# Optimization experiments

Measured on AMD Instinct MI355X. Metric: run time of the kernel, lower is better.

Reference implementation:

```python
import jax, jax.numpy as jnp
import numpy as np

B, T, D = 1, 2048, 1024
H = 16
HD = D // H
K = 4
FF = 4 * D
LAYERS = 24
EPS = 1.1920929e-07  # torch.finfo(float32).eps, RMSNorm default


def setup_inputs() -> dict:
    key = jax.random.key(0)
    ks = jax.random.split(key, 16)
    s = 0.02
    return {
        "x": jax.random.normal(ks[0], (B, T, D), jnp.float32),
        "gamma": jax.random.uniform(ks[1], (D,), jnp.float32),
        "beta": jax.random.normal(ks[2], (D,), jnp.float32) * 0.1,
        "iter_scale": jax.random.uniform(ks[3], (1,), jnp.float32),
        "qkv_bases": jax.random.normal(ks[4], (K, 3 * D, D), jnp.float32) * s,
        "o_bases": jax.random.normal(ks[5], (K, D, D), jnp.float32) * s,
        "gate_bases": jax.random.normal(ks[6], (K, FF, D), jnp.float32) * s,
        "up_bases": jax.random.normal(ks[7], (K, FF, D), jnp.float32) * s,
        "down_bases": jax.random.normal(ks[8], (K, D, FF), jnp.float32) * s,
        "alpha_qkv": jax.random.normal(ks[9], (LAYERS, K), jnp.float32) * 0.1 + jnp.eye(LAYERS, K)[:, :K] * 0.0 + jnp.concatenate([jnp.ones((LAYERS, 1)), jnp.zeros((LAYERS, K - 1))], axis=1),
        "alpha_o": jnp.concatenate([jnp.ones((LAYERS, 1)), jnp.zeros((LAYERS, K - 1))], axis=1) + jax.random.normal(ks[10], (LAYERS, K)) * 0.1,
        "alpha_gate": jnp.concatenate([jnp.ones((LAYERS, 1)), jnp.zeros((LAYERS, K - 1))], axis=1) + jax.random.normal(ks[11], (LAYERS, K)) * 0.1,
        "alpha_up": jnp.concatenate([jnp.ones((LAYERS, 1)), jnp.zeros((LAYERS, K - 1))], axis=1) + jax.random.normal(ks[12], (LAYERS, K)) * 0.1,
        "alpha_down": jnp.concatenate([jnp.ones((LAYERS, 1)), jnp.zeros((LAYERS, K - 1))], axis=1) + jax.random.normal(ks[13], (LAYERS, K)) * 0.1,
        "norm1_w": jnp.ones((D,), jnp.float32),
        "norm2_w": jnp.ones((D,), jnp.float32),
        "layer_idx": 5,
    }


def _rmsnorm(x, w):
    return x * jax.lax.rsqrt(jnp.mean(x * x, axis=-1, keepdims=True) + EPS) * w


def reference(x, gamma, beta, iter_scale, qkv_bases, o_bases, gate_bases, up_bases,
              down_bases, alpha_qkv, alpha_o, alpha_gate, alpha_up, alpha_down,
              norm1_w, norm2_w, layer_idx):
    Bx, Tx, Dx = x.shape
    # --- attention sub-block ---
    h = _rmsnorm(x, norm1_w) * gamma + beta
    W_qkv = jnp.einsum('k,kij->ij', alpha_qkv[layer_idx], qkv_bases)  # [3D, D]
    qkv = jnp.einsum('btd,od->bto', h, W_qkv).reshape(Bx, Tx, 3, H, HD)
    qkv = jnp.transpose(qkv, (2, 0, 3, 1, 4))  # [3, B, H, T, HD]
    q, k, v = qkv[0], qkv[1], qkv[2]
    scores = jnp.einsum('bhqd,bhkd->bhqk', q, k) / jnp.sqrt(jnp.asarray(HD, x.dtype))
    causal = jnp.tril(jnp.ones((Tx, Tx), bool))
    scores = jnp.where(causal, scores, jnp.asarray(-jnp.inf, scores.dtype))
    attn = jax.nn.softmax(scores, axis=-1)
    out = jnp.einsum('bhqk,bhkd->bhqd', attn, v)
    out = jnp.transpose(out, (0, 2, 1, 3)).reshape(Bx, Tx, Dx)
    W_o = jnp.einsum('k,kij->ij', alpha_o[layer_idx], o_bases)
    x_attn = x + jnp.einsum('btd,od->bto', out, W_o)
    # --- SwiGLU FFN sub-block ---
    h2 = _rmsnorm(x_attn, norm2_w) * gamma + beta
    W_g = jnp.einsum('k,kij->ij', alpha_gate[layer_idx], gate_bases)
    W_u = jnp.einsum('k,kij->ij', alpha_up[layer_idx], up_bases)
    W_d = jnp.einsum('k,kij->ij', alpha_down[layer_idx], down_bases)
    gate = jnp.einsum('btd,fd->btf', h2, W_g)
    up = jnp.einsum('btd,fd->btf', h2, W_u)
    ffn_out = jnp.einsum('btf,df->btd', jax.nn.silu(gate) * up, W_d)
    block_out = x_attn + ffn_out
    return x + (block_out - x) * iter_scale
```

## Files before the change

kernel.cpp:

```cpp
#include <hip/hip_runtime.h>
#include <hip/hip_bf16.h>
#include <math.h>

typedef __bf16 bf16;
typedef __bf16 bf16x8 __attribute__((ext_vector_type(8)));
typedef __bf16 bf16x4 __attribute__((ext_vector_type(4)));
typedef float f32x4 __attribute__((ext_vector_type(4)));

#define EPSc 1.1920929e-07f
#define LOG2E 1.44269504f

static __device__ __forceinline__ void glds16(const void* g, void* l) {
  __builtin_amdgcn_global_load_lds((const __attribute__((address_space(1))) void*)g,
                                   (__attribute__((address_space(3))) void*)l, 16, 0, 0);
}

static __device__ __forceinline__ bf16x4 comb4(const float* b0, const float* b1,
                                               const float* b2, const float* b3,
                                               float a0, float a1, float a2, float a3) {
  float4 v0 = *(const float4*)b0, v1 = *(const float4*)b1;
  float4 v2 = *(const float4*)b2, v3 = *(const float4*)b3;
  bf16x4 o;
  o[0] = (bf16)(a0*v0.x + a1*v1.x + a2*v2.x + a3*v3.x);
  o[1] = (bf16)(a0*v0.y + a1*v1.y + a2*v2.y + a3*v3.y);
  o[2] = (bf16)(a0*v0.z + a1*v1.z + a2*v2.z + a3*v3.z);
  o[3] = (bf16)(a0*v0.w + a1*v1.w + a2*v2.w + a3*v3.w);
  return o;
}

__global__ __launch_bounds__(256)
void prep1(const float* __restrict__ qkv_b, const float* __restrict__ a_qkv,
           const float* __restrict__ o_b,   const float* __restrict__ a_o,
           const float* __restrict__ x, const float* __restrict__ n1w,
           const float* __restrict__ gamma, const float* __restrict__ beta,
           const int* __restrict__ lidx,
           bf16* __restrict__ Wqkv, bf16* __restrict__ Wo, bf16* __restrict__ hbuf) {
  const int bid = blockIdx.x, tid = threadIdx.x;
  if (bid < 4096) {
    int li = lidx[0];
    const float* base; const float* al; bf16* out; size_t flat, n;
    if (bid < 3072) { base = qkv_b; al = a_qkv; out = Wqkv; flat = (size_t)bid << 10; n = (size_t)3072*1024; }
    else            { base = o_b;   al = a_o;   out = Wo;   flat = (size_t)(bid-3072) << 10; n = (size_t)1024*1024; }
    float a0 = al[li*4], a1 = al[li*4+1], a2 = al[li*4+2], a3 = al[li*4+3];
    size_t off = flat + tid*4;
    bf16x4 o = comb4(base+off, base+n+off, base+2*n+off, base+3*n+off, a0, a1, a2, a3);
    *(bf16x4*)&out[off] = o;
  } else {
    int row = bid - 4096, t = tid;
    const float4* xr = (const float4*)(x + (size_t)row*1024);
    float4 v = xr[t];
    float ss = v.x*v.x + v.y*v.y + v.z*v.z + v.w*v.w;
    #pragma unroll
    for (int off = 32; off > 0; off >>= 1) ss += __shfl_down(ss, off, 64);
    __shared__ float red[4];
    if ((t & 63) == 0) red[t >> 6] = ss;
    __syncthreads();
    float tot = red[0] + red[1] + red[2] + red[3];
    float r = rsqrtf(tot * (1.0f/1024.0f) + EPSc);
    float4 wv = ((const float4*)n1w)[t];
    float4 gv = ((const float4*)gamma)[t];
    float4 bv = ((const float4*)beta)[t];
    bf16x4 o;
    o[0] = (bf16)(v.x*r*wv.x*gv.x + bv.x);
    o[1] = (bf16)(v.y*r*wv.y*gv.y + bv.y);
    o[2] = (bf16)(v.z*r*wv.z*gv.z + bv.z);
    o[3] = (bf16)(v.w*r*wv.w*gv.w + bv.w);
    *(bf16x4*)&hbuf[(size_t)row*1024 + t*4] = o;
  }
}

__global__ __launch_bounds__(256) void rmsnorm_k(const float* __restrict__ x,
                                                 const float* __restrict__ w,
                                                 const float* __restrict__ gamma,
                                                 const float* __restrict__ beta,
                                                 bf16* __restrict__ out) {
  int row = blockIdx.x, t = threadIdx.x;
  const float4* xr = (const float4*)(x + (size_t)row*1024);
  float4 v = xr[t];
  float ss = v.x*v.x + v.y*v.y + v.z*v.z + v.w*v.w;
  #pragma unroll
  for (int off = 32; off > 0; off >>= 1) ss += __shfl_down(ss, off, 64);
  __shared__ float red[4];
  if ((t & 63) == 0) red[t >> 6] = ss;
  __syncthreads();
  float tot = red[0] + red[1] + red[2] + red[3];
  float r = rsqrtf(tot * (1.0f/1024.0f) + EPSc);
  float4 wv = ((const float4*)w)[t];
  float4 gv = ((const float4*)gamma)[t];
  float4 bv = ((const float4*)beta)[t];
  bf16x4 o;
  o[0] = (bf16)(v.x*r*wv.x*gv.x + bv.x);
  o[1] = (bf16)(v.y*r*wv.y*gv.y + bv.y);
  o[2] = (bf16)(v.z*r*wv.z*gv.z + bv.z);
  o[3] = (bf16)(v.w*r*wv.w*gv.w + bv.w);
  *(bf16x4*)&out[(size_t)row*1024 + t*4] = o;
}

template<int EP, int NTW>
__global__ __launch_bounds__(256)
void gemm_bt(const bf16* __restrict__ A, const bf16* __restrict__ Bw,
             int M, int N, int K, int lda, int ldb, int gx,
             float* __restrict__ outf, bf16* __restrict__ outb,
             const float* __restrict__ auxf, const float* __restrict__ auxf2,
             const float* __restrict__ iscale) {
  constexpr int BN = NTW * 32;
  __shared__ __align__(16) bf16 As[2][128*64];
  __shared__ __align__(16) bf16 Bs[2][BN*64];
  const int nwg = gridDim.x;
  const int orig = blockIdx.x;
  const int wg = (orig & 7) * (nwg >> 3) + (orig >> 3);
  const int tn0 = (wg % gx) * BN, tm0 = (wg / gx) * 128;
  const int tid = threadIdx.x, wave = tid >> 6, lane = tid & 63;
  const int lr = lane & 15, lg = lane >> 4;
  const int wr = wave >> 1, wc = wave & 1;
  f32x4 acc[4][NTW] = {};
  const int rs = lane >> 3;
  const int sc = (((lane & 7) ^ rs) << 3);
  const int x0 = ((lg ^ (lr & 7)) << 3);
  const int x1 = (((4 + lg) ^ (lr & 7)) << 3);

  const bf16* Abase = A + (size_t)tm0 * lda;
  const bf16* Bbase = Bw + (size_t)tn0 * ldb;

  auto stage = [&](bf16* as, bf16* bs, int k0) {
    #pragma unroll
    for (int j = 0; j < 4; ++j) {
      int chunk = wave*4 + j;
      int r = chunk*8 + rs;
      glds16(Abase + (size_t)r*lda + k0 + sc, as + chunk*512 + lane*8);
    }
    #pragma unroll
    for (int j = 0; j < NTW; ++j) {
      int chunk = wave*NTW + j;
      int r = chunk*8 + rs;
      glds16(Bbase + (size_t)r*ldb + k0 + sc, bs + chunk*512 + lane*8);
    }
  };
  auto comp = [&](const bf16* as, const bf16* bs) {
    #pragma unroll
    for (int kk = 0; kk < 2; ++kk) {
      const int x = kk ? x1 : x0;
      bf16x8 av[4], bv[NTW];
      #pragma unroll
      for (int m = 0; m < 4; ++m) av[m] = *(const bf16x8*)&as[(wr*64 + m*16 + lr)*64 + x];
      #pragma unroll
      for (int n = 0; n < NTW; ++n) bv[n] = *(const bf16x8*)&bs[(wc*NTW*16 + n*16 + lr)*64 + x];
      #pragma unroll
      for (int m = 0; m < 4; ++m)
        #pragma unroll
        for (int n = 0; n < NTW; ++n)
          acc[m][n] = __builtin_amdgcn_mfma_f32_16x16x32_bf16(av[m], bv[n], acc[m][n], 0, 0, 0);
    }
  };

  bf16 *a0 = As[0], *a1 = As[1], *b0 = Bs[0], *b1 = Bs[1];
  stage(a0, b0, 0);
  __syncthreads();
  for (int k0 = 64; k0 < K; k0 += 64) {
    stage(a1, b1, k0);
    comp(a0, b0);
    __syncthreads();
    bf16* t;
    t = a0; a0 = a1; a1 = t;
    t = b0; b0 = b1; b1 = t;
  }
  comp(a0, b0);

  float its = 0.f;
  if constexpr (EP == 4) its = iscale[0];
  #pragma unroll
  for (int m = 0; m < 4; ++m)
    #pragma unroll
    for (int n = 0; n < NTW; ++n)
      #pragma unroll
      for (int i = 0; i < 4; ++i) {
        int row = tm0 + wr*64 + m*16 + lg*4 + i;
        int col = tn0 + wc*NTW*16 + n*16 + lr;
        size_t idx = (size_t)row * N + col;
        float v = acc[m][n][i];
        if constexpr (EP == 0) outb[idx] = (bf16)v;
        else if constexpr (EP == 1) outf[idx] = auxf[idx] + v;
        else if constexpr (EP == 4) {
          float xv = auxf[idx], xa = auxf2[idx];
          outf[idx] = xv + (xa + v - xv) * its;
        }
      }
}

__global__ __launch_bounds__(512, 2)
void gemm_gu256(const bf16* __restrict__ A, const bf16* __restrict__ Bw,
                bf16* __restrict__ outb) {
  __shared__ __align__(16) bf16 L[2][2][2][8192];
  const int orig = blockIdx.x;
  const int wg = (orig & 7) * 32 + (orig >> 3);
  const int tn0 = (wg & 31) * 256, tm0 = (wg >> 5) * 256;
  const int tid = threadIdx.x, wave = tid >> 6, lane = tid & 63;
  const int lr = lane & 15, lg = lane >> 4;
  const int wr = wave >> 2, wn = wave & 3;
  const int rs8 = lane >> 3;
  const int gc8 = (((lane & 7) ^ rs8) << 3);
  const int xk0 = ((lg ^ (lr & 7)) << 3);
  const int xk1 = (((4 + lg) ^ (lr & 7)) << 3);
  f32x4 acc[8][4] = {};

  const bf16* Ab = A + (size_t)tm0 * 1024;
  const bf16* Bb = Bw + (size_t)tn0 * 1024;

  auto stage_half = [&](bf16* dst, const bf16* gbase, int half, int k0) {
    #pragma unroll
    for (int l = 0; l < 2; ++l) {
      int r = half*128 + (wave*2 + l)*8 + rs8;
      glds16(gbase + (size_t)r*1024 + k0 + gc8, dst + (wave*2 + l)*512 + lane*8);
    }
  };

  stage_half(&L[0][0][0][0], Ab, 0, 0);
  stage_half(&L[0][0][1][0], Ab, 1, 0);
  stage_half(&L[0][1][0][0], Bb, 0, 0);
  stage_half(&L[0][1][1][0], Bb, 1, 0);
  stage_half(&L[1][1][0][0], Bb, 0, 64);
  stage_half(&L[1][1][1][0], Bb, 1, 64);
  asm volatile("s_waitcnt vmcnt(4)" ::: "memory");
  __builtin_amdgcn_s_barrier();

  for (int t = 0; t < 16; ++t) {
    const int b = t & 1;
    const bf16* ah = &L[b][0][wr][0];
    const bf16* bh = &L[b][1][wn >> 1][0];
    bf16x8 breg[4][2];
    #pragma unroll
    for (int p = 0; p < 4; ++p) {
      if (p == 0) {
        #pragma unroll
        for (int n = 0; n < 4; ++n) {
          int row = (wn & 1)*64 + n*16 + lr;
          breg[n][0] = *(const bf16x8*)&bh[row*64 + xk0];
          breg[n][1] = *(const bf16x8*)&bh[row*64 + xk1];
        }
      }
      bf16x8 av[2][2];
      #pragma unroll
      for (int mi = 0; mi < 2; ++mi) {
        int row = p*32 + mi*16 + lr;
        av[mi][0] = *(const bf16x8*)&ah[row*64 + xk0];
        av[mi][1] = *(const bf16x8*)&ah[row*64 + xk1];
      }
      if (p == 0 && t < 15) stage_half(&L[b^1][0][0][0], Ab, 0, (t+1)*64);
      if (p == 1 && t < 15) stage_half(&L[b^1][0][1][0], Ab, 1, (t+1)*64);
      if (p == 2 && t < 14) stage_half(&L[b][1][0][0], Bb, 0, (t+2)*64);
      if (p == 3 && t < 14) stage_half(&L[b][1][1][0], Bb, 1, (t+2)*64);
      __builtin_amdgcn_s_barrier();
      __builtin_amdgcn_s_setprio(1);
      #pragma unroll
      for (int mi = 0; mi < 2; ++mi)
        #pragma unroll
        for (int n = 0; n < 4; ++n) {
          acc[p*2+mi][n] = __builtin_amdgcn_mfma_f32_16x16x32_bf16(av[mi][0], breg[n][0], acc[p*2+mi][n], 0, 0, 0);
          acc[p*2+mi][n] = __builtin_amdgcn_mfma_f32_16x16x32_bf16(av[mi][1], breg[n][1], acc[p*2+mi][n], 0, 0, 0);
        }
      __builtin_amdgcn_s_setprio(0);
      if (p == 3) {
        if (t >= 14) asm volatile("s_waitcnt vmcnt(0)" ::: "memory");
        else         asm volatile("s_waitcnt vmcnt(4)" ::: "memory");
      }
      __builtin_amdgcn_s_barrier();
    }
  }

  #pragma unroll
  for (int mf = 0; mf < 8; ++mf)
    #pragma unroll
    for (int j = 0; j < 2; ++j)
      #pragma unroll
      for (int i = 0; i < 4; ++i) {
        int row = tm0 + wr*128 + mf*16 + lg*4 + i;
        int col = (tn0 >> 1) + wn*32 + j*16 + lr;
        float g = acc[mf][2*j][i], u = acc[mf][2*j+1][i];
        float s = g / (1.f + __builtin_amdgcn_exp2f(-g * LOG2E));
        outb[(size_t)row * 4096 + col] = (bf16)(s * u);
      }
}

__global__ __launch_bounds__(256)
void attn_mega(const bf16* __restrict__ qkv, bf16* __restrict__ out,
               const float* __restrict__ gate_b, const float* __restrict__ up_b,
               const float* __restrict__ down_b,
               const float* __restrict__ a_gate, const float* __restrict__ a_up,
               const float* __restrict__ a_down, const int* __restrict__ lidx,
               bf16* __restrict__ Wgu, bf16* __restrict__ Wd) {
  __shared__ __align__(16) bf16 Ks[2][64*72];
  __shared__ __align__(16) bf16 Vt[2][64*66];
  __shared__ __align__(16) bf16 Ps[4][2][16*72];
  const int bid = blockIdx.x;
  const int tid = threadIdx.x;

  if (bid < 256) {
    const int cb = bid;
    int li = lidx[0];
    float g0 = a_gate[li*4], g1 = a_gate[li*4+1], g2 = a_gate[li*4+2], g3 = a_gate[li*4+3];
    float u0 = a_up[li*4],   u1 = a_up[li*4+1],   u2 = a_up[li*4+2],   u3 = a_up[li*4+3];
    float d0 = a_down[li*4], d1 = a_down[li*4+1], d2 = a_down[li*4+2], d3 = a_down[li*4+3];
    const size_t PS = (size_t)4096 * 1024;
    for (int it = 0; it < 48; ++it) {
      int chunk = it * 256 + cb;
      if (chunk < 8192) {
        int r = chunk, w = r & 31;
        int f = ((r >> 5) << 4) + (w & 15);
        const float* base = (w < 16) ? gate_b : up_b;
        float a0 = (w < 16) ? g0 : u0, a1 = (w < 16) ? g1 : u1;
        float a2 = (w < 16) ? g2 : u2, a3 = (w < 16) ? g3 : u3;
        size_t src = (size_t)f*1024 + tid*4;
        bf16x4 o = comb4(base+src, base+PS+src, base+2*PS+src, base+3*PS+src, a0, a1, a2, a3);
        *(bf16x4*)&Wgu[((size_t)r << 10) + tid*4] = o;
      } else {
        size_t off = ((size_t)(chunk - 8192) << 10) + tid*4;
        bf16x4 o = comb4(down_b+off, down_b+PS+off, down_b+2*PS+off, down_b+3*PS+off, d0, d1, d2, d3);
        *(bf16x4*)&Wd[off] = o;
      }
    }
    return;
  }

  const int a = bid - 256;
  const int qb = 15 - (a >> 4);
  const int h = a & 15;
  const int wave = tid >> 6, lane = tid & 63;
  const int lr = lane & 15, lg = lane >> 4;
  const int q0 = qb * 128;
  const int qw = q0 + wave * 32;

  bf16x8 qf[2][2];
  #pragma unroll
  for (int qt = 0; qt < 2; ++qt) {
    const bf16* qrow = qkv + (size_t)(qw + qt*16 + lr)*3072 + h*64;
    qf[qt][0] = *(const bf16x8*)(qrow + lg*8);
    qf[qt][1] = *(const bf16x8*)(qrow + 32 + lg*8);
  }
  f32x4 o[2][4] = {};
  float mrow[2], lrow[2];
  mrow[0] = mrow[1] = -__builtin_inff();
  lrow[0] = lrow[1] = 0.f;
  const int xsrc = (lane & 48) | (lg << 2);

  const int r0 = tid >> 3, r1 = r0 + 32;
  const int c0 = (tid & 7) << 3;
  const bf16* kb = qkv + 1024 + h*64 + c0;
  const bf16* vb = qkv + 2048 + h*64 + c0;

  bf16x8 kreg[2], vreg[2];
  auto stage_load = [&](int kv0) {
    kreg[0] = *(const bf16x8*)(kb + (size_t)(kv0 + r0)*3072);
    kreg[1] = *(const bf16x8*)(kb + (size_t)(kv0 + r1)*3072);
    vreg[0] = *(const bf16x8*)(vb + (size_t)(kv0 + r0)*3072);
    vreg[1] = *(const bf16x8*)(vb + (size_t)(kv0 + r1)*3072);
  };
  auto stage_write = [&](int buf) {
    *(bf16x8*)&Ks[buf][r0*72 + c0] = kreg[0];
    *(bf16x8*)&Ks[buf][r1*72 + c0] = kreg[1];
    #pragma unroll
    for (int e = 0; e < 8; ++e) Vt[buf][(c0 + e)*66 + r0] = vreg[0][e];
    #pragma unroll
    for (int e = 0; e < 8; ++e) Vt[buf][(c0 + e)*66 + r1] = vreg[1][e];
  };

  stage_load(0);
  stage_write(0);
  __syncthreads();
  int cur = 0;

  const float C = 0.125f * LOG2E;
  const int nt = 2 * (qb + 1);

  for (int t = 0; t < nt; ++t) {
    const int kv0 = t * 64;
    if (t < nt-1) stage_load(kv0 + 64);

    f32x4 s[2][4] = {};
    __builtin_amdgcn_s_setprio(1);
    #pragma unroll
    for (int n = 0; n < 4; ++n) {
      bf16x8 k0f = *(const bf16x8*)&Ks[cur][(n*16 + lr)*72 + lg*8];
      bf16x8 k1f = *(const bf16x8*)&Ks[cur][(n*16 + lr)*72 + 32 + lg*8];
      #pragma unroll
      for (int qt = 0; qt < 2; ++qt) {
        s[qt][n] = __builtin_amdgcn_mfma_f32_16x16x32_bf16(k0f, qf[qt][0], s[qt][n], 0, 0, 0);
        s[qt][n] = __builtin_amdgcn_mfma_f32_16x16x32_bf16(k1f, qf[qt][1], s[qt][n], 0, 0, 0);
      }
    }
    __builtin_amdgcn_s_setprio(0);

    if (kv0 + 63 > qw) {
      #pragma unroll
      for (int qt = 0; qt < 2; ++qt) {
        const int qv = qw + qt*16 + lr;
        #pragma unroll
        for (int n = 0; n < 4; ++n)
          #pragma unroll
          for (int i = 0; i < 4; ++i)
            if (kv0 + n*16 + lg*4 + i > qv) s[qt][n][i] = -__builtin_inff();
      }
    }

    float pmn[2];
    #pragma unroll
    for (int qt = 0; qt < 2; ++qt) {
      f32x4 t0 = s[qt][0], t1 = s[qt][1];
      #pragma unroll
      for (int i = 0; i < 4; ++i) { t0[i] = fmaxf(t0[i], s[qt][2][i]); t1[i] = fmaxf(t1[i], s[qt][3][i]); }
      float a0 = fmaxf(t0[0], t0[1]), a1 = fmaxf(t0[2], t0[3]);
      float b0 = fmaxf(t1[0], t1[1]), b1 = fmaxf(t1[2], t1[3]);
      float mnew = fmaxf(fmaxf(a0, a1), fmaxf(b0, b1));
      mnew = fmaxf(mnew, __shfl_xor(mnew, 16, 64));
      mnew = fmaxf(mnew, __shfl_xor(mnew, 32, 64));
      pmn[qt] = mnew * C;
    }
    bool grow = (pmn[0] > mrow[0] + 8.f) || (pmn[1] > mrow[1] + 8.f);
    if (__any(grow)) {
      #pragma unroll
      for (int qt = 0; qt < 2; ++qt) {
        float mt = fmaxf(mrow[qt], pmn[qt]);
        float fc = __builtin_amdgcn_exp2f(mrow[qt] - mt);
        mrow[qt] = mt;
        lrow[qt] *= fc;
        #pragma unroll
        for (int i = 0; i < 4; ++i) {
          float fci = __shfl(fc, xsrc + i, 64);
          #pragma unroll
          for (int nd = 0; nd < 4; ++nd) o[qt][nd][i] *= fci;
        }
      }
    }
    #pragma unroll
    for (int qt = 0; qt < 2; ++qt) {
      float mref = fmaxf(mrow[qt], -3e38f);
      float rsum = 0.f;
      #pragma unroll
      for (int n = 0; n < 4; ++n) {
        bf16x4 p4;
        #pragma unroll
        for (int i = 0; i < 4; ++i) {
          float e = __builtin_amdgcn_exp2f(__builtin_fmaf(s[qt][n][i], C, -mref));
          rsum += e;
          p4[i] = (bf16)e;
        }
        *(bf16x4*)&Ps[wave][qt][lr*72 + n*16 + lg*4] = p4;
      }
      rsum += __shfl_xor(rsum, 16, 64);
      rsum += __shfl_xor(rsum, 32, 64);
      lrow[qt] += rsum;
    }
    asm volatile("s_waitcnt lgkmcnt(0)" ::: "memory");

    #pragma unroll
    for (int kk = 0; kk < 2; ++kk) {
      bf16x8 pf0 = *(const bf16x8*)&Ps[wave][0][lr*72 + kk*32 + lg*8];
      bf16x8 pf1 = *(const bf16x8*)&Ps[wave][1][lr*72 + kk*32 + lg*8];
      __builtin_amdgcn_s_setprio(1);
      #pragma unroll
      for (int nd = 0; nd < 4; ++nd) {
        bf16x8 vf = *(const bf16x8*)&Vt[cur][(nd*16 + lr)*66 + kk*32 + lg*8];
        o[0][nd] = __builtin_amdgcn_mfma_f32_16x16x32_bf16(pf0, vf, o[0][nd], 0, 0, 0);
        o[1][nd] = __builtin_amdgcn_mfma_f32_16x16x32_bf16(pf1, vf, o[1][nd], 0, 0, 0);
      }
      __builtin_amdgcn_s_setprio(0);
    }
    if (t < nt-1) {
      stage_write(cur ^ 1);
      __syncthreads();
      cur ^= 1;
    }
  }
  #pragma unroll
  for (int qt = 0; qt < 2; ++qt)
    #pragma unroll
    for (int i = 0; i < 4; ++i) {
      float li = __shfl(lrow[qt], xsrc + i, 64);
      float inv = 1.f / li;
      #pragma unroll
      for (int nd = 0; nd < 4; ++nd)
        out[(size_t)(qw + qt*16 + lg*4 + i)*1024 + h*64 + nd*16 + lr] = (bf16)(o[qt][nd][i]*inv);
    }
}

extern "C" void kernel_launch(void* const* d_in, const int* in_sizes, int n_in,
                              void* d_out, int out_size, void* d_ws, size_t ws_size,
                              hipStream_t stream) {
  const float* x        = (const float*)d_in[0];
  const float* gamma    = (const float*)d_in[1];
  const float* beta     = (const float*)d_in[2];
  const float* iscale   = (const float*)d_in[3];
  const float* qkv_b    = (const float*)d_in[4];
  const float* o_b      = (const float*)d_in[5];
  const float* gate_b   = (const float*)d_in[6];
  const float* up_b     = (const float*)d_in[7];
  const float* down_b   = (const float*)d_in[8];
  const float* a_qkv    = (const float*)d_in[9];
  const float* a_o      = (const float*)d_in[10];
  const float* a_gate   = (const float*)d_in[11];
  const float* a_up     = (const float*)d_in[12];
  const float* a_down   = (const float*)d_in[13];
  const float* n1w      = (const float*)d_in[14];
  const float* n2w      = (const float*)d_in[15];
  const int*   lidx     = (const int*)d_in[16];

  char* p = (char*)d_ws;
  auto alloc = [&](size_t bytes) { char* r = p; p += (bytes + 255) & ~(size_t)255; return r; };
  bf16*  Wqkv = (bf16*)alloc((size_t)3072*1024*2);
  bf16*  Wo   = (bf16*)alloc((size_t)1024*1024*2);
  bf16*  Wgu  = (bf16*)alloc((size_t)8192*1024*2);
  bf16*  Wd   = (bf16*)alloc((size_t)1024*4096*2);
  bf16*  hbuf = (bf16*)alloc((size_t)2048*1024*2);
  bf16*  qkvb = (bf16*)alloc((size_t)2048*3072*2);
  bf16*  attn = (bf16*)alloc((size_t)2048*1024*2);
  float* xat  = (float*)alloc((size_t)2048*1024*4);
  bf16*  h2   = (bf16*)alloc((size_t)2048*1024*2);
  bf16*  act  = (bf16*)alloc((size_t)2048*4096*2);
  float* out  = (float*)d_out;

  prep1<<<6144, 256, 0, stream>>>(qkv_b, a_qkv, o_b, a_o, x, n1w, gamma, beta, lidx,
                                  Wqkv, Wo, hbuf);
  gemm_bt<0,4><<<24*16, 256, 0, stream>>>(hbuf, Wqkv, 2048, 3072, 1024, 1024, 1024, 24,
                                          nullptr, qkvb, nullptr, nullptr, nullptr);
  attn_mega<<<512, 256, 0, stream>>>(qkvb, attn, gate_b, up_b, down_b,
                                     a_gate, a_up, a_down, lidx, Wgu, Wd);
  gemm_bt<1,2><<<16*16, 256, 0, stream>>>(attn, Wo, 2048, 1024, 1024, 1024, 1024, 16,
                                          xat, nullptr, x, nullptr, nullptr);
  rmsnorm_k<<<2048, 256, 0, stream>>>(xat, n2w, gamma, beta, h2);
  gemm_gu256<<<256, 512, 0, stream>>>(h2, Wgu, act);
  gemm_bt<4,2><<<16*16, 256, 0, stream>>>(act, Wd, 2048, 1024, 4096, 4096, 4096, 16,
                                          out, nullptr, x, xat, iscale);
}
```

Measured before the change: 201.7 us.

## Split causal attention KV range in two and merge partials in new kernel

Each attention (query-block, head) work item is split into two halves of the key/value range, doubling the attention block count so heavy causal query blocks are spread over more CUs. Each half writes unnormalised fp32 outputs plus its running max and sum, and a new merge kernel combines them into the bf16 attention output. The P tile stride in LDS also changes from 72 to 68, which changes the bank mapping. In exchange this adds an extra launch and fp32 partial traffic of roughly 16 MB written and read back, and the split is even in tiles rather than in causal work.

```diff
diff --git a/kernel.cpp b/kernel.cpp
--- a/kernel.cpp
+++ b/kernel.cpp
@@ -282,15 +282,41 @@
 }
 
 __global__ __launch_bounds__(256)
-void attn_mega(const bf16* __restrict__ qkv, bf16* __restrict__ out,
+void attn_merge(const float* __restrict__ oPart, const float* __restrict__ mPart,
+                const float* __restrict__ lPart, bf16* __restrict__ out) {
+  const int q = blockIdx.x, tid = threadIdx.x;
+  const int h = tid >> 4;
+  const size_t HQ = (size_t)16 * 2048;
+  float mA = mPart[h*2048 + q],      mB = mPart[HQ + h*2048 + q];
+  float lA = lPart[h*2048 + q],      lB = lPart[HQ + h*2048 + q];
+  float fm = fmaxf(mA, mB);
+  float eA = __builtin_amdgcn_exp2f(mA - fm);
+  float eB = __builtin_amdgcn_exp2f(mB - fm);
+  float inv = 1.f / (lA*eA + lB*eB);
+  const size_t QD = (size_t)2048 * 1024;
+  size_t idx = (size_t)q*1024 + tid*4;
+  float4 oA = *(const float4*)&oPart[idx];
+  float4 oB = *(const float4*)&oPart[QD + idx];
+  bf16x4 o;
+  o[0] = (bf16)((oA.x*eA + oB.x*eB) * inv);
+  o[1] = (bf16)((oA.y*eA + oB.y*eB) * inv);
+  o[2] = (bf16)((oA.z*eA + oB.z*eB) * inv);
+  o[3] = (bf16)((oA.w*eA + oB.w*eB) * inv);
+  *(bf16x4*)&out[idx] = o;
+}
+
+__global__ __launch_bounds__(256)
+void attn_mega(const bf16* __restrict__ qkv,
                const float* __restrict__ gate_b, const float* __restrict__ up_b,
                const float* __restrict__ down_b,
                const float* __restrict__ a_gate, const float* __restrict__ a_up,
                const float* __restrict__ a_down, const int* __restrict__ lidx,
-               bf16* __restrict__ Wgu, bf16* __restrict__ Wd) {
+               bf16* __restrict__ Wgu, bf16* __restrict__ Wd,
+               float* __restrict__ oPart, float* __restrict__ mPart,
+               float* __restrict__ lPart) {
   __shared__ __align__(16) bf16 Ks[2][64*72];
   __shared__ __align__(16) bf16 Vt[2][64*66];
-  __shared__ __align__(16) bf16 Ps[4][2][16*72];
+  __shared__ __align__(16) bf16 Ps[4][2][16*68];
   const int bid = blockIdx.x;
   const int tid = threadIdx.x;
 
@@ -322,12 +348,15 @@
   }
 
   const int a = bid - 256;
-  const int qb = 15 - (a >> 4);
-  const int h = a & 15;
+  const int sp = a >> 8;
+  const int rem = a & 255;
+  const int qb = 15 - (rem >> 4);
+  const int h = rem & 15;
   const int wave = tid >> 6, lane = tid & 63;
   const int lr = lane & 15, lg = lane >> 4;
   const int q0 = qb * 128;
   const int qw = q0 + wave * 32;
+  const int t0 = sp * (qb + 1), t1 = t0 + (qb + 1);
 
   bf16x8 qf[2][2];
   #pragma unroll
@@ -363,17 +392,16 @@
     for (int e = 0; e < 8; ++e) Vt[buf][(c0 + e)*66 + r1] = vreg[1][e];
   };
 
-  stage_load(0);
+  stage_load(t0 * 64);
   stage_write(0);
   __syncthreads();
   int cur = 0;
 
   const float C = 0.125f * LOG2E;
-  const int nt = 2 * (qb + 1);
-
-  for (int t = 0; t < nt; ++t) {
+
+  for (int t = t0; t < t1; ++t) {
     const int kv0 = t * 64;
-    if (t < nt-1) stage_load(kv0 + 64);
+    if (t < t1-1) stage_load(kv0 + 64);
 
     f32x4 s[2][4] = {};
     __builtin_amdgcn_s_setprio(1);
@@ -404,11 +432,11 @@
     float pmn[2];
     #pragma unroll
     for (int qt = 0; qt < 2; ++qt) {
-      f32x4 t0 = s[qt][0], t1 = s[qt][1];
-      #pragma unroll
-      for (int i = 0; i < 4; ++i) { t0[i] = fmaxf(t0[i], s[qt][2][i]); t1[i] = fmaxf(t1[i], s[qt][3][i]); }
-      float a0 = fmaxf(t0[0], t0[1]), a1 = fmaxf(t0[2], t0[3]);
-      float b0 = fmaxf(t1[0], t1[1]), b1 = fmaxf(t1[2], t1[3]);
+      f32x4 u0 = s[qt][0], u1 = s[qt][1];
+      #pragma unroll
+      for (int i = 0; i < 4; ++i) { u0[i] = fmaxf(u0[i], s[qt][2][i]); u1[i] = fmaxf(u1[i], s[qt][3][i]); }
+      float a0 = fmaxf(u0[0], u0[1]), a1 = fmaxf(u0[2], u0[3]);
+      float b0 = fmaxf(u1[0], u1[1]), b1 = fmaxf(u1[2], u1[3]);
       float mnew = fmaxf(fmaxf(a0, a1), fmaxf(b0, b1));
       mnew = fmaxf(mnew, __shfl_xor(mnew, 16, 64));
       mnew = fmaxf(mnew, __shfl_xor(mnew, 32, 64));
@@ -443,7 +471,7 @@
           rsum += e;
           p4[i] = (bf16)e;
         }
-        *(bf16x4*)&Ps[wave][qt][lr*72 + n*16 + lg*4] = p4;
+        *(bf16x4*)&Ps[wave][qt][lr*68 + n*16 + lg*4] = p4;
       }
       rsum += __shfl_xor(rsum, 16, 64);
       rsum += __shfl_xor(rsum, 32, 64);
@@ -453,8 +481,8 @@
 
     #pragma unroll
     for (int kk = 0; kk < 2; ++kk) {
-      bf16x8 pf0 = *(const bf16x8*)&Ps[wave][0][lr*72 + kk*32 + lg*8];
-      bf16x8 pf1 = *(const bf16x8*)&Ps[wave][1][lr*72 + kk*32 + lg*8];
+      bf16x8 pf0 = *(const bf16x8*)&Ps[wave][0][lr*68 + kk*32 + lg*8];
+      bf16x8 pf1 = *(const bf16x8*)&Ps[wave][1][lr*68 + kk*32 + lg*8];
       __builtin_amdgcn_s_setprio(1);
       #pragma unroll
       for (int nd = 0; nd < 4; ++nd) {
@@ -464,22 +492,29 @@
       }
       __builtin_amdgcn_s_setprio(0);
     }
-    if (t < nt-1) {
+    if (t < t1-1) {
       stage_write(cur ^ 1);
       __syncthreads();
       cur ^= 1;
     }
   }
+
+  float* oP = oPart + (size_t)sp * 2048 * 1024;
   #pragma unroll
-  for (int qt = 0; qt < 2; ++qt)
+  for (int qt = 0; qt < 2; ++qt) {
     #pragma unroll
     for (int i = 0; i < 4; ++i) {
-      float li = __shfl(lrow[qt], xsrc + i, 64);
-      float inv = 1.f / li;
+      size_t row = (size_t)(qw + qt*16 + lg*4 + i)*1024 + h*64;
       #pragma unroll
       for (int nd = 0; nd < 4; ++nd)
-        out[(size_t)(qw + qt*16 + lg*4 + i)*1024 + h*64 + nd*16 + lr] = (bf16)(o[qt][nd][i]*inv);
-    }
+        oP[row + nd*16 + lr] = o[qt][nd][i];
+    }
+    if (lane < 16) {
+      size_t si = (size_t)sp * 16 * 2048 + (size_t)h * 2048 + qw + qt*16 + lr;
+      mPart[si] = mrow[qt];
+      lPart[si] = lrow[qt];
+    }
+  }
 }
 
 extern "C" void kernel_launch(void* const* d_in, const int* in_sizes, int n_in,
@@ -515,14 +550,19 @@
   float* xat  = (float*)alloc((size_t)2048*1024*4);
   bf16*  h2   = (bf16*)alloc((size_t)2048*1024*2);
   bf16*  act  = (bf16*)alloc((size_t)2048*4096*2);
+  float* oPart = (float*)alloc((size_t)2*2048*1024*4);
+  float* mPart = (float*)alloc((size_t)2*16*2048*4);
+  float* lPart = (float*)alloc((size_t)2*16*2048*4);
   float* out  = (float*)d_out;
 
   prep1<<<6144, 256, 0, stream>>>(qkv_b, a_qkv, o_b, a_o, x, n1w, gamma, beta, lidx,
                                   Wqkv, Wo, hbuf);
   gemm_bt<0,4><<<24*16, 256, 0, stream>>>(hbuf, Wqkv, 2048, 3072, 1024, 1024, 1024, 24,
                                           nullptr, qkvb, nullptr, nullptr, nullptr);
-  attn_mega<<<512, 256, 0, stream>>>(qkvb, attn, gate_b, up_b, down_b,
-                                     a_gate, a_up, a_down, lidx, Wgu, Wd);
+  attn_mega<<<768, 256, 0, stream>>>(qkvb, gate_b, up_b, down_b,
+                                     a_gate, a_up, a_down, lidx, Wgu, Wd,
+                                     oPart, mPart, lPart);
+  attn_merge<<<2048, 256, 0, stream>>>(oPart, mPart, lPart, attn);
   gemm_bt<1,2><<<16*16, 256, 0, stream>>>(attn, Wo, 2048, 1024, 1024, 1024, 1024, 16,
                                           xat, nullptr, x, nullptr, nullptr);
   rmsnorm_k<<<2048, 256, 0, stream>>>(xat, n2w, gamma, beta, h2);
```

Result: faster. 193.7 us (-4.0%).
